# Kernel tuning notes

Hardware: AMD Instinct MI355X
Metric: run time of the kernel (lower is better)

## Reference

```python
import jax, jax.numpy as jnp
import numpy as np
import math

B, N, DIM, H, D, M = 2, 2048, 512, 8, 64, 128  # batch, seq, model dim, heads, head_dim, num_features


def _sample_orf(head_dim, num_features, seed=0):
    """Orthogonal random features with chi(d) norm scaling (FAVOR+), numpy host-side."""
    rng = np.random.default_rng(seed)
    blocks = []
    while len(blocks) * head_dim < num_features:
        G = rng.standard_normal((head_dim, head_dim)).astype(np.float32)
        Q, _ = np.linalg.qr(G)
        norms = np.linalg.norm(rng.standard_normal((head_dim, head_dim)).astype(np.float32), axis=1)
        blocks.append(np.diag(norms) @ Q.T)
    return np.concatenate(blocks, axis=0)[:num_features]


def setup_inputs() -> dict:
    key = jax.random.key(0)
    ks = jax.random.split(key, 6)
    inner = H * D
    x = jax.random.normal(ks[0], (B, N, DIM), dtype=jnp.float32)
    s = DIM ** -0.5
    Wq = jax.random.normal(ks[1], (inner, DIM), dtype=jnp.float32) * s
    Wk = jax.random.normal(ks[2], (inner, DIM), dtype=jnp.float32) * s
    Wv = jax.random.normal(ks[3], (inner, DIM), dtype=jnp.float32) * s
    Wo = jax.random.normal(ks[4], (DIM, inner), dtype=jnp.float32) * (inner ** -0.5)
    bo = jax.random.normal(ks[5], (DIM,), dtype=jnp.float32) * 0.01
    omega = jnp.asarray(_sample_orf(D, M), dtype=jnp.float32)  # [M, D]
    return {"x": x, "omega": omega, "Wq": Wq, "Wk": Wk, "Wv": Wv, "Wo": Wo, "bo": bo}


def _phi(x, omega, is_query):
    # x: [B,H,N,D], omega: [M,D] -> [B,H,N,M]
    proj = jnp.einsum('bhnd,md->bhnm', x, omega)
    log_phi = proj - 0.5 * jnp.sum(x * x, axis=-1, keepdims=True)
    if is_query:
        log_phi = log_phi - jnp.max(log_phi, axis=-1, keepdims=True)
    else:
        log_phi = log_phi - jnp.max(log_phi)
    return jnp.exp(log_phi) / math.sqrt(M) + 1e-4


def reference(x, omega, Wq, Wk, Wv, Wo, bo):
    # projections: torch Linear is y = x @ W.T
    q = (x @ Wq.T).reshape(B, N, H, D).transpose(0, 2, 1, 3)  # [B,H,N,D]
    k = (x @ Wk.T).reshape(B, N, H, D).transpose(0, 2, 1, 3)
    v = (x @ Wv.T).reshape(B, N, H, D).transpose(0, 2, 1, 3)
    scale = D ** -0.25
    phi_q = _phi(q * scale, omega, True)   # [B,H,N,M]
    phi_k = _phi(k * scale, omega, False)  # [B,H,N,M]

    # Causal linear attention as a recurrent scan over the sequence; math equals
    # cumsum of einsum('bhnm,bhnd->bhnmd') without the O(N*M*D) intermediate.
    def step(carry, inp):
        kv, ksum = carry                      # [B,H,M,D], [B,H,M]
        pqn, pkn, vn = inp                    # [B,H,M], [B,H,M], [B,H,D]
        kv = kv + pkn[..., None] * vn[:, :, None, :]
        ksum = ksum + pkn
        o = jnp.einsum('bhm,bhmd->bhd', pqn, kv)
        z = 1.0 / (jnp.einsum('bhm,bhm->bh', pqn, ksum) + 1e-6)
        return (kv, ksum), o * z[..., None]

    init = (jnp.zeros((B, H, M, D), x.dtype), jnp.zeros((B, H, M), x.dtype))
    xs = (phi_q.transpose(2, 0, 1, 3), phi_k.transpose(2, 0, 1, 3), v.transpose(2, 0, 1, 3))
    _, outs = jax.lax.scan(step, init, xs)    # outs: [N,B,H,D]
    out = outs.transpose(1, 0, 2, 3).reshape(B, N, H * D)
    return out @ Wo.T + bo
```

## Files before the change

### kernel.cpp

```cpp
#include <hip/hip_runtime.h>
#include <math.h>

#define B_ 2
#define N_ 2048
#define DIM_ 512
#define H_ 8
#define D_ 64
#define M_ 128
#define NC_ 32
#define C_ 64

#define INV_SQRT_M 0.08838834764831845f
#define QK_SCALE 0.35355339059327373f

typedef __attribute__((ext_vector_type(8))) short bf16x8;
typedef __attribute__((ext_vector_type(4))) short bf16x4;
typedef __attribute__((ext_vector_type(4))) float f32x4;

#define MFMA16(a, b, c) __builtin_amdgcn_mfma_f32_16x16x32_bf16((a), (b), (c), 0, 0, 0)

__device__ __forceinline__ short f2bf(float f) {
    union { float f; unsigned u; } x; x.f = f;
    unsigned r = (x.u + 0x7FFFu + ((x.u >> 16) & 1u)) >> 16;
    return (short)r;
}
__device__ __forceinline__ float bf2f(short s) {
    union { unsigned u; float f; } x; x.u = ((unsigned)(unsigned short)s) << 16;
    return x.f;
}
__device__ __forceinline__ unsigned encf(float f) {
    unsigned u = __float_as_uint(f);
    return (u & 0x80000000u) ? ~u : (u | 0x80000000u);
}
__device__ __forceinline__ float decf(unsigned e) {
    unsigned u = (e & 0x80000000u) ? (e & 0x7FFFFFFFu) : ~e;
    return __uint_as_float(u);
}

__device__ __forceinline__ void gl16(void* lds, const void* g) {
    __builtin_amdgcn_global_load_lds(
        (const __attribute__((address_space(1))) unsigned int*)g,
        (__attribute__((address_space(3))) unsigned int*)lds,
        16, 0, 0);
}

__device__ __forceinline__ bf16x8 ld_frag(const short* base, int row0, int k0, int ldk) {
    const int lane = threadIdx.x & 63;
    return *(const bf16x8*)(base + (row0 + (lane & 15)) * ldk + k0 + ((lane >> 4) << 3));
}
__device__ __forceinline__ bf16x8 ld_fragT(const short* base, int col0, int k0, int ldk) {
    const int lane = threadIdx.x & 63;
    const short* p = base + (k0 + ((lane >> 4) << 3)) * ldk + col0 + (lane & 15);
    bf16x8 r;
    #pragma unroll
    for (int i = 0; i < 8; ++i) r[i] = p[i * ldk];
    return r;
}

__global__ __launch_bounds__(256) void prep(
    const float* __restrict__ x, const float* __restrict__ Wq, const float* __restrict__ Wk,
    const float* __restrict__ Wv, const float* __restrict__ Wo,
    short* __restrict__ xh, short* __restrict__ xl,
    short* __restrict__ Wch, short* __restrict__ Woh, unsigned* __restrict__ gmaxu)
{
    int i4 = blockIdx.x * 256 + threadIdx.x;
    if (i4 == 0) gmaxu[0] = 0u;
    if (i4 < 524288) {
        float4 v = *(const float4*)(x + (size_t)i4 * 4);
        float a[4] = {v.x, v.y, v.z, v.w};
        bf16x4 hi, lo;
        #pragma unroll
        for (int u = 0; u < 4; ++u) {
            short h = f2bf(a[u]); hi[u] = h; lo[u] = f2bf(a[u] - bf2f(h));
        }
        *(bf16x4*)(xh + (size_t)i4 * 4) = hi;
        *(bf16x4*)(xl + (size_t)i4 * 4) = lo;
    } else {
        int r = i4 - 524288;
        int widx = r >> 16, off4 = r & 65535;
        const float* src; short* dst; float sc;
        if (widx == 0)      { src = Wq; dst = Wch;          sc = QK_SCALE; }
        else if (widx == 1) { src = Wk; dst = Wch + 262144; sc = QK_SCALE; }
        else if (widx == 2) { src = Wv; dst = Wch + 524288; sc = 1.f; }
        else                { src = Wo; dst = Woh;          sc = 1.f; }
        float4 v = *(const float4*)(src + (size_t)off4 * 4);
        bf16x4 hi;
        hi[0] = f2bf(v.x * sc); hi[1] = f2bf(v.y * sc);
        hi[2] = f2bf(v.z * sc); hi[3] = f2bf(v.w * sc);
        *(bf16x4*)(dst + (size_t)off4 * 4) = hi;
    }
}

__global__ __launch_bounds__(256) void prep_omw(const float* __restrict__ omega,
    const float* __restrict__ Wq, const float* __restrict__ Wk,
    short* __restrict__ Wch, short* __restrict__ Wcl)
{
    __shared__ float Ws[64][65];
    __shared__ float om[128][64];
    const int t = threadIdx.x;
    const int qk = blockIdx.x >> 6, h = (blockIdx.x >> 3) & 7, cb = blockIdx.x & 7;
    const int col0 = cb * 64;
    const float* W = qk ? Wk : Wq;
    for (int i = t; i < 64 * 64; i += 256) {
        int d = i >> 6, c = i & 63;
        Ws[d][c] = W[(size_t)(h * 64 + d) * 512 + col0 + c] * QK_SCALE;
    }
    for (int i = t; i < 128 * 64; i += 256) om[i >> 6][i & 63] = omega[i];
    __syncthreads();
    const int lane = t & 63, w = t >> 6;
    const int c = col0 + lane;
    float Wcol[64];
    #pragma unroll
    for (int d = 0; d < 64; ++d) Wcol[d] = Ws[d][lane];
    for (int mi = 0; mi < 32; ++mi) {
        int m = w * 32 + mi;
        float acc = 0.f;
        #pragma unroll
        for (int d = 0; d < 64; d += 4) {
            float4 o4 = *(const float4*)&om[m][d];
            acc += o4.x * Wcol[d] + o4.y * Wcol[d+1] + o4.z * Wcol[d+2] + o4.w * Wcol[d+3];
        }
        int row = 1536 + qk * 1024 + h * 128 + m;
        short hi = f2bf(acc);
        Wch[(size_t)row * 512 + c] = hi;
        Wcl[(size_t)row * 512 + c] = f2bf(acc - bf2f(hi));
    }
}

__global__ __launch_bounds__(256) void gemm_fused(
    const short* __restrict__ xh, const short* __restrict__ xl,
    const short* __restrict__ Wch, const short* __restrict__ Wcl,
    float* __restrict__ projq, float* __restrict__ projk,
    short* __restrict__ vbf, float* __restrict__ ssqbuf,
    float* __restrict__ qmaxp, float* __restrict__ pmaxp)
{
    __shared__ short Ah[128 * 32];
    __shared__ short Al[128 * 32];
    __shared__ short Bh[128 * 32];
    __shared__ short Bl[128 * 32];
    const int t = threadIdx.x, lane = t & 63, wave = t >> 6;
    const int wr = wave >> 1, wc = wave & 1;
    const int row0 = blockIdx.x * 128;
    const int by = blockIdx.y;
    const int col0 = by * 128;
    const int l_row = lane >> 2, l_col = (lane & 3) << 3;
    const bool three = (by >= 12);
    f32x4 acc[4][4];
    #pragma unroll
    for (int m = 0; m < 4; ++m)
        #pragma unroll
        for (int n = 0; n < 4; ++n) { f32x4 z = {0.f, 0.f, 0.f, 0.f}; acc[m][n] = z; }
    for (int k0 = 0; k0 < 512; k0 += 32) {
        #pragma unroll
        for (int sub = 0; sub < 2; ++sub) {
            int s = wave * 2 + sub;
            int gr = s * 16 + l_row;
            size_t ga = (size_t)(row0 + gr) * 512 + k0 + l_col;
            size_t gb = (size_t)(col0 + gr) * 512 + k0 + l_col;
            gl16(&Ah[s * 512], xh + ga);
            gl16(&Bh[s * 512], Wch + gb);
            if (three) {
                gl16(&Al[s * 512], xl + ga);
                gl16(&Bl[s * 512], Wcl + gb);
            }
        }
        __syncthreads();
        if (three) {
            bf16x8 bh[4], bl[4];
            #pragma unroll
            for (int n = 0; n < 4; ++n) {
                bh[n] = ld_frag(Bh, wc * 64 + n * 16, 0, 32);
                bl[n] = ld_frag(Bl, wc * 64 + n * 16, 0, 32);
            }
            #pragma unroll
            for (int m = 0; m < 4; ++m) {
                bf16x8 ah = ld_frag(Ah, wr * 64 + m * 16, 0, 32);
                bf16x8 al = ld_frag(Al, wr * 64 + m * 16, 0, 32);
                #pragma unroll
                for (int n = 0; n < 4; ++n) {
                    acc[m][n] = MFMA16(al, bh[n], acc[m][n]);
                    acc[m][n] = MFMA16(ah, bl[n], acc[m][n]);
                    acc[m][n] = MFMA16(ah, bh[n], acc[m][n]);
                }
            }
        } else {
            bf16x8 bh[4];
            #pragma unroll
            for (int n = 0; n < 4; ++n) bh[n] = ld_frag(Bh, wc * 64 + n * 16, 0, 32);
            #pragma unroll
            for (int m = 0; m < 4; ++m) {
                bf16x8 ah = ld_frag(Ah, wr * 64 + m * 16, 0, 32);
                #pragma unroll
                for (int n = 0; n < 4; ++n) acc[m][n] = MFMA16(ah, bh[n], acc[m][n]);
            }
        }
        __syncthreads();
    }
    if (by < 8) {
        const int qk = by >> 2;
        const int head = (by * 2 + wc) & 7;
        #pragma unroll
        for (int m = 0; m < 4; ++m)
            #pragma unroll
            for (int i = 0; i < 4; ++i) {
                float s = 0.f;
                #pragma unroll
                for (int n = 0; n < 4; ++n) { float v2 = acc[m][n][i]; s += v2 * v2; }
                s += __shfl_xor(s, 1); s += __shfl_xor(s, 2);
                s += __shfl_xor(s, 4); s += __shfl_xor(s, 8);
                if ((lane & 15) == 0) {
                    int row = row0 + wr * 64 + m * 16 + ((lane >> 4) << 2) + i;
                    int b = row >> 11, nn = row & 2047;
                    ssqbuf[qk * 32768 + (b * 8 + head) * 2048 + nn] = s;
                }
            }
    } else if (by < 12) {
        #pragma unroll
        for (int m = 0; m < 4; ++m)
            #pragma unroll
            for (int n = 0; n < 4; ++n)
                #pragma unroll
                for (int i = 0; i < 4; ++i) {
                    int row = row0 + wr * 64 + m * 16 + ((lane >> 4) << 2) + i;
                    int gc = col0 + wc * 64 + n * 16 + (lane & 15);
                    int c = gc - 1024, h = c >> 6, d = c & 63;
                    int b = row >> 11, nn = row & 2047;
                    vbf[((size_t)(b * 8 + h) * 2048 + nn) * 64 + d] = f2bf(acc[m][n][i]);
                }
    } else {
        float* dst = (by < 20) ? projq : projk;
        float* mdst = (by < 20) ? qmaxp : pmaxp;
        const int coff = (by < 20) ? 1536 : 2560;
        const int h = (by < 20) ? (by - 12) : (by - 20);
        #pragma unroll
        for (int m = 0; m < 4; ++m)
            #pragma unroll
            for (int n = 0; n < 4; ++n)
                #pragma unroll
                for (int i = 0; i < 4; ++i) {
                    int row = row0 + wr * 64 + m * 16 + ((lane >> 4) << 2) + i;
                    int pc = col0 - coff + wc * 64 + n * 16 + (lane & 15);
                    dst[(size_t)row * 1024 + pc] = acc[m][n][i];
                }
        #pragma unroll
        for (int m = 0; m < 4; ++m)
            #pragma unroll
            for (int i = 0; i < 4; ++i) {
                float mx = fmaxf(fmaxf(acc[m][0][i], acc[m][1][i]),
                                 fmaxf(acc[m][2][i], acc[m][3][i]));
                mx = fmaxf(mx, __shfl_xor(mx, 1));
                mx = fmaxf(mx, __shfl_xor(mx, 2));
                mx = fmaxf(mx, __shfl_xor(mx, 4));
                mx = fmaxf(mx, __shfl_xor(mx, 8));
                if ((lane & 15) == 0) {
                    int row = row0 + wr * 64 + m * 16 + ((lane >> 4) << 2) + i;
                    int b = row >> 11, nn = row & 2047;
                    size_t g = (size_t)(b * 8 + h) * 2048 + nn;
                    mdst[2 * g + wc] = mx;
                }
            }
    }
}

__global__ __launch_bounds__(256) void kmax_reduce(const float* __restrict__ pmaxp,
    const float* __restrict__ ssqbuf, unsigned* __restrict__ gmaxu)
{
    float m = -3.402823466e38f;
    for (int g = blockIdx.x * 256 + threadIdx.x; g < 32768; g += 8192)
        m = fmaxf(m, fmaxf(pmaxp[2 * g], pmaxp[2 * g + 1]) - 0.5f * ssqbuf[32768 + g]);
    #pragma unroll
    for (int off = 1; off < 64; off <<= 1) m = fmaxf(m, __shfl_xor(m, off));
    __shared__ float w[4];
    if ((threadIdx.x & 63) == 0) w[threadIdx.x >> 6] = m;
    __syncthreads();
    if (threadIdx.x == 0)
        atomicMax(gmaxu, encf(fmaxf(fmaxf(w[0], w[1]), fmaxf(w[2], w[3]))));
}

__global__ __launch_bounds__(256) void phi_q_ew(
    const float* __restrict__ projq, const float* __restrict__ qmaxp,
    short* __restrict__ phiq)
{
    size_t i4 = (size_t)blockIdx.x * 256 + threadIdx.x;
    size_t e = i4 * 4;
    int r = (int)(e >> 10), c = (int)(e & 1023);
    int h = c >> 7, m = c & 127;
    int b = r >> 11, n = r & 2047;
    int g = (b * 8 + h) * 2048 + n;
    float4 p = *(const float4*)(projq + e);
    float qm = fmaxf(qmaxp[2 * (size_t)g], qmaxp[2 * (size_t)g + 1]);
    bf16x4 o;
    o[0] = f2bf(expf(p.x - qm) * INV_SQRT_M + 1e-4f);
    o[1] = f2bf(expf(p.y - qm) * INV_SQRT_M + 1e-4f);
    o[2] = f2bf(expf(p.z - qm) * INV_SQRT_M + 1e-4f);
    o[3] = f2bf(expf(p.w - qm) * INV_SQRT_M + 1e-4f);
    *(bf16x4*)(phiq + (size_t)g * 128 + m) = o;
}

__global__ __launch_bounds__(256) void chunk_kv_mfma(
    const float* __restrict__ projk, const float* __restrict__ ssqbuf,
    const unsigned* __restrict__ gmaxu, const short* __restrict__ v_bf,
    short* __restrict__ phik, float* __restrict__ S, float* __restrict__ ksum)
{
    __shared__ short pk_l[64][136];
    __shared__ short v_l[64][72];
    const int t = threadIdx.x, lane = t & 63, wave = t >> 6;
    const int wr = wave >> 1, wc = wave & 1;
    const int bh = blockIdx.x >> 5, j = blockIdx.x & 31;
    const int b = bh >> 3, h = bh & 7;
    const int n0 = j << 6;
    const float g = decf(gmaxu[0]);
    #pragma unroll
    for (int it = 0; it < 8; ++it) {
        int e4 = t + it * 256;
        int r = e4 >> 5, c4 = (e4 & 31) << 2;
        float4 p = *(const float4*)(projk + ((size_t)(b * 2048 + n0 + r)) * 1024 + h * 128 + c4);
        float skv = 0.5f * ssqbuf[32768 + bh * 2048 + n0 + r];
        bf16x4 o;
        o[0] = f2bf(expf(p.x - skv - g) * INV_SQRT_M + 1e-4f);
        o[1] = f2bf(expf(p.y - skv - g) * INV_SQRT_M + 1e-4f);
        o[2] = f2bf(expf(p.z - skv - g) * INV_SQRT_M + 1e-4f);
        o[3] = f2bf(expf(p.w - skv - g) * INV_SQRT_M + 1e-4f);
        *(bf16x4*)&pk_l[r][c4] = o;
        *(bf16x4*)(phik + ((size_t)(bh * 2048 + n0 + r)) * 128 + c4) = o;
    }
    #pragma unroll
    for (int it = 0; it < 2; ++it) {
        int idx = t + it * 256;
        int r = idx >> 3, c8 = (idx & 7) << 3;
        *(bf16x8*)&v_l[r][c8] = *(const bf16x8*)(v_bf + ((size_t)(bh * 2048 + n0 + r)) * 64 + c8);
    }
    __syncthreads();
    f32x4 acc[2][4];
    #pragma unroll
    for (int mi = 0; mi < 2; ++mi)
        #pragma unroll
        for (int ni = 0; ni < 4; ++ni) { f32x4 z = {0.f, 0.f, 0.f, 0.f}; acc[mi][ni] = z; }
    #pragma unroll
    for (int ks = 0; ks < 2; ++ks) {
        bf16x8 a0 = ld_fragT(&v_l[0][0], wr * 32, ks * 32, 72);
        bf16x8 a1 = ld_fragT(&v_l[0][0], wr * 32 + 16, ks * 32, 72);
        #pragma unroll
        for (int ni = 0; ni < 4; ++ni) {
            bf16x8 bb = ld_fragT(&pk_l[0][0], wc * 64 + ni * 16, ks * 32, 136);
            acc[0][ni] = MFMA16(a0, bb, acc[0][ni]);
            acc[1][ni] = MFMA16(a1, bb, acc[1][ni]);
        }
    }
    const size_t sbase = ((size_t)blockIdx.x) << 13;
    #pragma unroll
    for (int mi = 0; mi < 2; ++mi)
        #pragma unroll
        for (int ni = 0; ni < 4; ++ni)
            #pragma unroll
            for (int i = 0; i < 4; ++i) {
                int row = wr * 32 + mi * 16 + ((lane >> 4) << 2) + i;
                int col = wc * 64 + ni * 16 + (lane & 15);
                S[sbase + (size_t)row * 128 + col] = acc[mi][ni][i];
            }
    if (t < 128) {
        float s = 0.f;
        #pragma unroll 8
        for (int n = 0; n < 64; ++n) s += bf2f(pk_l[n][t]);
        ksum[((size_t)blockIdx.x) * 128 + t] = s;
    }
}

__global__ __launch_bounds__(256) void prefix_scan(const float* __restrict__ S,
    const float* __restrict__ ksum, short* __restrict__ STbf, float* __restrict__ kpre)
{
    const int bh = blockIdx.x, y = blockIdx.y, t = threadIdx.x;
    if (y < 32) {
        int e = y * 256 + t;
        size_t base = (size_t)bh * NC_ * 8192 + e;
        float vals[NC_];
        #pragma unroll
        for (int j = 0; j < NC_; ++j) vals[j] = S[base + (size_t)j * 8192];
        float run = 0.f;
        #pragma unroll
        for (int j = 0; j < NC_; ++j) {
            STbf[base + (size_t)j * 8192] = f2bf(run);
            run += vals[j];
        }
    } else if (t < 128) {
        size_t base = (size_t)bh * NC_ * 128 + t;
        float vals[NC_];
        #pragma unroll
        for (int j = 0; j < NC_; ++j) vals[j] = ksum[base + (size_t)j * 128];
        float run = 0.f;
        #pragma unroll
        for (int j = 0; j < NC_; ++j) {
            kpre[base + (size_t)j * 128] = run;
            run += vals[j];
        }
    }
}

__global__ __launch_bounds__(256) void chunk_out_mfma(
    const short* __restrict__ phi_q, const short* __restrict__ phi_k,
    const short* __restrict__ v_bf, const short* __restrict__ STbf,
    const float* __restrict__ kpre, short* __restrict__ o_hi, short* __restrict__ o_lo)
{
    __shared__ short pq_l[64][136];
    __shared__ short pkst_l[64][136];
    __shared__ short v_l[64][72];
    __shared__ short a_l[64][72];
    __shared__ float rsum[64][8];
    __shared__ float den[64];
    __shared__ float ksp_l[128];
    const int t = threadIdx.x, lane = t & 63, wave = t >> 6;
    const int wr = wave >> 1, wc = wave & 1;
    const int bh = blockIdx.x >> 5, j = blockIdx.x & 31;
    const int n0 = j << 6;
    const size_t prow = (size_t)bh * N_ + n0;
    #pragma unroll
    for (int it = 0; it < 4; ++it) {
        int idx = t + it * 256;
        int r = idx >> 4, c8 = (idx & 15) << 3;
        *(bf16x8*)&pq_l[r][c8] = *(const bf16x8*)(phi_q + (prow + r) * 128 + c8);
        *(bf16x8*)&pkst_l[r][c8] = *(const bf16x8*)(phi_k + (prow + r) * 128 + c8);
    }
    #pragma unroll
    for (int it = 0; it < 2; ++it) {
        int idx = t + it * 256;
        int r = idx >> 3, c8 = (idx & 7) << 3;
        *(bf16x8*)&v_l[r][c8] = *(const bf16x8*)(v_bf + (prow + r) * 64 + c8);
    }
    if (t < 128) ksp_l[t] = kpre[((size_t)bh * NC_ + j) * 128 + t];
    __syncthreads();
    f32x4 qk[2][2];
    #pragma unroll
    for (int mi = 0; mi < 2; ++mi)
        #pragma unroll
        for (int ni = 0; ni < 2; ++ni) { f32x4 z = {0.f, 0.f, 0.f, 0.f}; qk[mi][ni] = z; }
    #pragma unroll
    for (int ks = 0; ks < 4; ++ks) {
        bf16x8 a0 = ld_frag(&pq_l[0][0], wr * 32, ks * 32, 136);
        bf16x8 a1 = ld_frag(&pq_l[0][0], wr * 32 + 16, ks * 32, 136);
        bf16x8 b0 = ld_frag(&pkst_l[0][0], wc * 32, ks * 32, 136);
        bf16x8 b1 = ld_frag(&pkst_l[0][0], wc * 32 + 16, ks * 32, 136);
        qk[0][0] = MFMA16(a0, b0, qk[0][0]);
        qk[0][1] = MFMA16(a0, b1, qk[0][1]);
        qk[1][0] = MFMA16(a1, b0, qk[1][0]);
        qk[1][1] = MFMA16(a1, b1, qk[1][1]);
    }
    #pragma unroll
    for (int mi = 0; mi < 2; ++mi)
        #pragma unroll
        for (int i = 0; i < 4; ++i) {
            int row = wr * 32 + mi * 16 + ((lane >> 4) << 2) + i;
            float part = 0.f;
            #pragma unroll
            for (int ni = 0; ni < 2; ++ni) {
                int col = wc * 32 + ni * 16 + (lane & 15);
                float val = (col <= row) ? qk[mi][ni][i] : 0.f;
                a_l[row][col] = f2bf(val);
                part += val;
            }
            part += __shfl_xor(part, 1);
            part += __shfl_xor(part, 2);
            part += __shfl_xor(part, 4);
            part += __shfl_xor(part, 8);
            if ((lane & 15) == 0) rsum[row][wc] = part;
        }
    {
        int row = t & 63, qq = t >> 6;
        float s = 0.f;
        #pragma unroll
        for (int m = 0; m < 32; ++m) s += bf2f(pq_l[row][qq * 32 + m]) * ksp_l[qq * 32 + m];
        rsum[row][4 + qq] = s;
    }
    __syncthreads();
    #pragma unroll
    for (int it = 0; it < 4; ++it) {
        int idx = t + it * 256;
        int r = idx >> 4, c8 = (idx & 15) << 3;
        *(bf16x8*)&pkst_l[r][c8] =
            *(const bf16x8*)(STbf + (((size_t)bh * NC_ + j) << 13) + r * 128 + c8);
    }
    if (t < 64) {
        float s = rsum[t][0] + rsum[t][1] + rsum[t][4] + rsum[t][5] + rsum[t][6] + rsum[t][7];
        den[t] = 1.0f / (s + 1e-6f);
    }
    __syncthreads();
    f32x4 oa[2][2];
    #pragma unroll
    for (int mi = 0; mi < 2; ++mi)
        #pragma unroll
        for (int ni = 0; ni < 2; ++ni) { f32x4 z = {0.f, 0.f, 0.f, 0.f}; oa[mi][ni] = z; }
    #pragma unroll
    for (int ks = 0; ks < 2; ++ks) {
        bf16x8 a0 = ld_frag(&a_l[0][0], wr * 32, ks * 32, 72);
        bf16x8 a1 = ld_frag(&a_l[0][0], wr * 32 + 16, ks * 32, 72);
        #pragma unroll
        for (int ni = 0; ni < 2; ++ni) {
            bf16x8 bb = ld_fragT(&v_l[0][0], wc * 32 + ni * 16, ks * 32, 72);
            oa[0][ni] = MFMA16(a0, bb, oa[0][ni]);
            oa[1][ni] = MFMA16(a1, bb, oa[1][ni]);
        }
    }
    #pragma unroll
    for (int ks = 0; ks < 4; ++ks) {
        bf16x8 a0 = ld_frag(&pq_l[0][0], wr * 32, ks * 32, 136);
        bf16x8 a1 = ld_frag(&pq_l[0][0], wr * 32 + 16, ks * 32, 136);
        #pragma unroll
        for (int ni = 0; ni < 2; ++ni) {
            bf16x8 bb = ld_frag(&pkst_l[0][0], wc * 32 + ni * 16, ks * 32, 136);
            oa[0][ni] = MFMA16(a0, bb, oa[0][ni]);
            oa[1][ni] = MFMA16(a1, bb, oa[1][ni]);
        }
    }
    const int b_ = bh >> 3, h = bh & 7;
    #pragma unroll
    for (int mi = 0; mi < 2; ++mi)
        #pragma unroll
        for (int ni = 0; ni < 2; ++ni)
            #pragma unroll
            for (int i = 0; i < 4; ++i) {
                int row = wr * 32 + mi * 16 + ((lane >> 4) << 2) + i;
                int col = wc * 32 + ni * 16 + (lane & 15);
                float val = oa[mi][ni][i] * den[row];
                size_t oi = ((size_t)b_ * N_ + n0 + row) * 512 + h * 64 + col;
                short hi = f2bf(val);
                o_hi[oi] = hi;
                o_lo[oi] = f2bf(val - bf2f(hi));
            }
}

__global__ __launch_bounds__(256) void gemm_out(
    const short* __restrict__ ohi, const short* __restrict__ olo,
    const short* __restrict__ Woh, const float* __restrict__ bo, float* __restrict__ out)
{
    __shared__ short Ah[128 * 32];
    __shared__ short Al[128 * 32];
    __shared__ short Bh[64 * 32];
    const int t = threadIdx.x, lane = t & 63, wave = t >> 6;
    const int row0 = blockIdx.x * 128, col0 = blockIdx.y * 64;
    const int l_row = lane >> 2, l_col = (lane & 3) << 3;
    f32x4 acc[2][4];
    #pragma unroll
    for (int m = 0; m < 2; ++m)
        #pragma unroll
        for (int n = 0; n < 4; ++n) { f32x4 z = {0.f, 0.f, 0.f, 0.f}; acc[m][n] = z; }
    for (int k0 = 0; k0 < 512; k0 += 32) {
        #pragma unroll
        for (int sub = 0; sub < 2; ++sub) {
            int s = wave * 2 + sub;
            int gr = s * 16 + l_row;
            size_t ga = (size_t)(row0 + gr) * 512 + k0 + l_col;
            gl16(&Ah[s * 512], ohi + ga);
            gl16(&Al[s * 512], olo + ga);
        }
        {
            int gr = wave * 16 + l_row;
            size_t gb = (size_t)(col0 + gr) * 512 + k0 + l_col;
            gl16(&Bh[wave * 512], Woh + gb);
        }
        __syncthreads();
        bf16x8 bh[4];
        #pragma unroll
        for (int n = 0; n < 4; ++n) bh[n] = ld_frag(Bh, n * 16, 0, 32);
        #pragma unroll
        for (int m = 0; m < 2; ++m) {
            bf16x8 ah = ld_frag(Ah, wave * 32 + m * 16, 0, 32);
            bf16x8 al = ld_frag(Al, wave * 32 + m * 16, 0, 32);
            #pragma unroll
            for (int n = 0; n < 4; ++n) {
                acc[m][n] = MFMA16(al, bh[n], acc[m][n]);
                acc[m][n] = MFMA16(ah, bh[n], acc[m][n]);
            }
        }
        __syncthreads();
    }
    #pragma unroll
    for (int m = 0; m < 2; ++m)
        #pragma unroll
        for (int n = 0; n < 4; ++n)
            #pragma unroll
            for (int i = 0; i < 4; ++i) {
                int gr = row0 + wave * 32 + m * 16 + ((lane >> 4) << 2) + i;
                int gc = col0 + n * 16 + (lane & 15);
                out[(size_t)gr * 512 + gc] = acc[m][n][i] + bo[gc];
            }
}

extern "C" void kernel_launch(void* const* d_in, const int* in_sizes, int n_in,
                              void* d_out, int out_size, void* d_ws, size_t ws_size,
                              hipStream_t stream) {
    const float* x     = (const float*)d_in[0];
    const float* omega = (const float*)d_in[1];
    const float* Wq    = (const float*)d_in[2];
    const float* Wk    = (const float*)d_in[3];
    const float* Wv    = (const float*)d_in[4];
    const float* Wo    = (const float*)d_in[5];
    const float* bo    = (const float*)d_in[6];
    float* out = (float*)d_out;

    char* w = (char*)d_ws;
    short* xh   = (short*)(w);
    short* xl   = (short*)(w + (4ull  << 20));
    short* Wch  = (short*)(w + (8ull  << 20));
    short* Wcl  = (short*)(w + (11ull << 20) + (512ull << 10));
    short* Woh  = (short*)(w + (16ull << 20));
    float* projq= (float*)(w + (17ull << 20));
    float* projk= (float*)(w + (33ull << 20));
    short* vbf  = (short*)(w + (49ull << 20));
    short* STbf = (short*)(w + (53ull << 20));
    short* ohi  = (short*)(w + (61ull << 20));
    short* olo  = (short*)(w + (65ull << 20));
    float* ssqb = (float*)(w + (69ull << 20));
    float* ksum = (float*)(w + (69ull << 20) + (256ull << 10));
    float* kpre = (float*)(w + (69ull << 20) + (512ull << 10));
    float* pmaxp= (float*)(w + (69ull << 20) + (768ull << 10));
    float* qmaxp= (float*)(w + (70ull << 20));
    unsigned* gmaxu = (unsigned*)(w + (70ull << 20) + (256ull << 10));
    short* phiq = (short*)(w);
    short* phik = (short*)(w + (8ull << 20));
    float* S    = projq;

    prep<<<3072, 256, 0, stream>>>(x, Wq, Wk, Wv, Wo, xh, xl, Wch, Woh, gmaxu);
    prep_omw<<<128, 256, 0, stream>>>(omega, Wq, Wk, Wch, Wcl);
    gemm_fused<<<dim3(32, 28), 256, 0, stream>>>(xh, xl, Wch, Wcl, projq, projk,
                                                 vbf, ssqb, qmaxp, pmaxp);
    kmax_reduce<<<32, 256, 0, stream>>>(pmaxp, ssqb, gmaxu);
    phi_q_ew<<<4096, 256, 0, stream>>>(projq, qmaxp, phiq);
    chunk_kv_mfma<<<512, 256, 0, stream>>>(projk, ssqb, gmaxu, vbf, phik, S, ksum);
    prefix_scan<<<dim3(16, 33), 256, 0, stream>>>(S, ksum, STbf, kpre);
    chunk_out_mfma<<<512, 256, 0, stream>>>(phiq, phik, vbf, STbf, kpre, ohi, olo);
    gemm_out<<<dim3(32, 8), 256, 0, stream>>>(ohi, olo, Woh, bo, out);
}
```

Measured before the change: 182.8 us.

## Fuse phi exponentials into projection GEMM epilogue and drop plain Q projection

The fused GEMM no longer computes the plain q projection, since only its omega-folded form is needed for phi_q. Its epilogue now applies the row-max exponential directly and writes bf16 phi_q and a per-row-normalised phi_k instead of fp32 projections, which removes the phi_q_ew kernel and the large fp32 intermediate traffic. The global key max is applied later as a per-row scale when phi_k is loaded in the chunk kernels, and the chunk KV states are stored as bf16. The rescale of an already-rounded bf16 value and the bf16 chunk states add rounding error in exchange for less memory traffic.

```diff
diff --git a/kernel.cpp b/kernel.cpp
--- a/kernel.cpp
+++ b/kernel.cpp
@@ -58,8 +58,8 @@
 }
 
 __global__ __launch_bounds__(256) void prep(
-    const float* __restrict__ x, const float* __restrict__ Wq, const float* __restrict__ Wk,
-    const float* __restrict__ Wv, const float* __restrict__ Wo,
+    const float* __restrict__ x, const float* __restrict__ Wk, const float* __restrict__ Wv,
+    const float* __restrict__ Wo,
     short* __restrict__ xh, short* __restrict__ xl,
     short* __restrict__ Wch, short* __restrict__ Woh, unsigned* __restrict__ gmaxu)
 {
@@ -75,13 +75,12 @@
         }
         *(bf16x4*)(xh + (size_t)i4 * 4) = hi;
         *(bf16x4*)(xl + (size_t)i4 * 4) = lo;
-    } else {
+    } else if (i4 < 720896) {
         int r = i4 - 524288;
         int widx = r >> 16, off4 = r & 65535;
         const float* src; short* dst; float sc;
-        if (widx == 0)      { src = Wq; dst = Wch;          sc = QK_SCALE; }
-        else if (widx == 1) { src = Wk; dst = Wch + 262144; sc = QK_SCALE; }
-        else if (widx == 2) { src = Wv; dst = Wch + 524288; sc = 1.f; }
+        if (widx == 0)      { src = Wk; dst = Wch;          sc = QK_SCALE; }
+        else if (widx == 1) { src = Wv; dst = Wch + 262144; sc = 1.f; }
         else                { src = Wo; dst = Woh;          sc = 1.f; }
         float4 v = *(const float4*)(src + (size_t)off4 * 4);
         bf16x4 hi;
@@ -120,7 +119,7 @@
             float4 o4 = *(const float4*)&om[m][d];
             acc += o4.x * Wcol[d] + o4.y * Wcol[d+1] + o4.z * Wcol[d+2] + o4.w * Wcol[d+3];
         }
-        int row = 1536 + qk * 1024 + h * 128 + m;
+        int row = 1024 + qk * 1024 + h * 128 + m;
         short hi = f2bf(acc);
         Wch[(size_t)row * 512 + c] = hi;
         Wcl[(size_t)row * 512 + c] = f2bf(acc - bf2f(hi));
@@ -130,21 +129,21 @@
 __global__ __launch_bounds__(256) void gemm_fused(
     const short* __restrict__ xh, const short* __restrict__ xl,
     const short* __restrict__ Wch, const short* __restrict__ Wcl,
-    float* __restrict__ projq, float* __restrict__ projk,
-    short* __restrict__ vbf, float* __restrict__ ssqbuf,
-    float* __restrict__ qmaxp, float* __restrict__ pmaxp)
+    short* __restrict__ phiq, short* __restrict__ pkloc,
+    short* __restrict__ vbf, float* __restrict__ ssqbuf, float* __restrict__ pmaxp)
 {
     __shared__ short Ah[128 * 32];
     __shared__ short Al[128 * 32];
     __shared__ short Bh[128 * 32];
     __shared__ short Bl[128 * 32];
+    __shared__ float rmx[128][2];
     const int t = threadIdx.x, lane = t & 63, wave = t >> 6;
     const int wr = wave >> 1, wc = wave & 1;
     const int row0 = blockIdx.x * 128;
     const int by = blockIdx.y;
     const int col0 = by * 128;
     const int l_row = lane >> 2, l_col = (lane & 3) << 3;
-    const bool three = (by >= 12);
+    const bool three = (by >= 8);
     f32x4 acc[4][4];
     #pragma unroll
     for (int m = 0; m < 4; ++m)
@@ -196,9 +195,8 @@
         }
         __syncthreads();
     }
-    if (by < 8) {
-        const int qk = by >> 2;
-        const int head = (by * 2 + wc) & 7;
+    if (by < 4) {
+        const int head = by * 2 + wc;
         #pragma unroll
         for (int m = 0; m < 4; ++m)
             #pragma unroll
@@ -211,10 +209,10 @@
                 if ((lane & 15) == 0) {
                     int row = row0 + wr * 64 + m * 16 + ((lane >> 4) << 2) + i;
                     int b = row >> 11, nn = row & 2047;
-                    ssqbuf[qk * 32768 + (b * 8 + head) * 2048 + nn] = s;
+                    ssqbuf[(b * 8 + head) * 2048 + nn] = s;
                 }
             }
-    } else if (by < 12) {
+    } else if (by < 8) {
         #pragma unroll
         for (int m = 0; m < 4; ++m)
             #pragma unroll
@@ -223,25 +221,13 @@
                 for (int i = 0; i < 4; ++i) {
                     int row = row0 + wr * 64 + m * 16 + ((lane >> 4) << 2) + i;
                     int gc = col0 + wc * 64 + n * 16 + (lane & 15);
-                    int c = gc - 1024, h = c >> 6, d = c & 63;
+                    int c = gc - 512, h = c >> 6, d = c & 63;
                     int b = row >> 11, nn = row & 2047;
                     vbf[((size_t)(b * 8 + h) * 2048 + nn) * 64 + d] = f2bf(acc[m][n][i]);
                 }
     } else {
-        float* dst = (by < 20) ? projq : projk;
-        float* mdst = (by < 20) ? qmaxp : pmaxp;
-        const int coff = (by < 20) ? 1536 : 2560;
-        const int h = (by < 20) ? (by - 12) : (by - 20);
-        #pragma unroll
-        for (int m = 0; m < 4; ++m)
-            #pragma unroll
-            for (int n = 0; n < 4; ++n)
-                #pragma unroll
-                for (int i = 0; i < 4; ++i) {
-                    int row = row0 + wr * 64 + m * 16 + ((lane >> 4) << 2) + i;
-                    int pc = col0 - coff + wc * 64 + n * 16 + (lane & 15);
-                    dst[(size_t)row * 1024 + pc] = acc[m][n][i];
-                }
+        const bool isq = (by < 16);
+        const int h = isq ? (by - 8) : (by - 16);
         #pragma unroll
         for (int m = 0; m < 4; ++m)
             #pragma unroll
@@ -252,12 +238,28 @@
                 mx = fmaxf(mx, __shfl_xor(mx, 2));
                 mx = fmaxf(mx, __shfl_xor(mx, 4));
                 mx = fmaxf(mx, __shfl_xor(mx, 8));
-                if ((lane & 15) == 0) {
-                    int row = row0 + wr * 64 + m * 16 + ((lane >> 4) << 2) + i;
-                    int b = row >> 11, nn = row & 2047;
-                    size_t g = (size_t)(b * 8 + h) * 2048 + nn;
-                    mdst[2 * g + wc] = mx;
+                if ((lane & 15) == 0)
+                    rmx[wr * 64 + m * 16 + ((lane >> 4) << 2) + i][wc] = mx;
+            }
+        __syncthreads();
+        short* dst = isq ? phiq : pkloc;
+        #pragma unroll
+        for (int m = 0; m < 4; ++m)
+            #pragma unroll
+            for (int i = 0; i < 4; ++i) {
+                int lr = wr * 64 + m * 16 + ((lane >> 4) << 2) + i;
+                float fm = fmaxf(rmx[lr][0], rmx[lr][1]);
+                int row = row0 + lr;
+                int b = row >> 11, nn = row & 2047;
+                size_t g = (size_t)(b * 8 + h) * 2048 + nn;
+                #pragma unroll
+                for (int n = 0; n < 4; ++n) {
+                    int mc = wc * 64 + n * 16 + (lane & 15);
+                    float e = expf(acc[m][n][i] - fm);
+                    float val = isq ? (e * INV_SQRT_M + 1e-4f) : e;
+                    dst[g * 128 + mc] = f2bf(val);
                 }
+                if (!isq && wc == 0 && (lane & 15) == 0) pmaxp[g] = fm;
             }
     }
 }
@@ -267,7 +269,7 @@
 {
     float m = -3.402823466e38f;
     for (int g = blockIdx.x * 256 + threadIdx.x; g < 32768; g += 8192)
-        m = fmaxf(m, fmaxf(pmaxp[2 * g], pmaxp[2 * g + 1]) - 0.5f * ssqbuf[32768 + g]);
+        m = fmaxf(m, pmaxp[g] - 0.5f * ssqbuf[g]);
     #pragma unroll
     for (int off = 1; off < 64; off <<= 1) m = fmaxf(m, __shfl_xor(m, off));
     __shared__ float w[4];
@@ -277,52 +279,34 @@
         atomicMax(gmaxu, encf(fmaxf(fmaxf(w[0], w[1]), fmaxf(w[2], w[3]))));
 }
 
-__global__ __launch_bounds__(256) void phi_q_ew(
-    const float* __restrict__ projq, const float* __restrict__ qmaxp,
-    short* __restrict__ phiq)
-{
-    size_t i4 = (size_t)blockIdx.x * 256 + threadIdx.x;
-    size_t e = i4 * 4;
-    int r = (int)(e >> 10), c = (int)(e & 1023);
-    int h = c >> 7, m = c & 127;
-    int b = r >> 11, n = r & 2047;
-    int g = (b * 8 + h) * 2048 + n;
-    float4 p = *(const float4*)(projq + e);
-    float qm = fmaxf(qmaxp[2 * (size_t)g], qmaxp[2 * (size_t)g + 1]);
-    bf16x4 o;
-    o[0] = f2bf(expf(p.x - qm) * INV_SQRT_M + 1e-4f);
-    o[1] = f2bf(expf(p.y - qm) * INV_SQRT_M + 1e-4f);
-    o[2] = f2bf(expf(p.z - qm) * INV_SQRT_M + 1e-4f);
-    o[3] = f2bf(expf(p.w - qm) * INV_SQRT_M + 1e-4f);
-    *(bf16x4*)(phiq + (size_t)g * 128 + m) = o;
-}
-
 __global__ __launch_bounds__(256) void chunk_kv_mfma(
-    const float* __restrict__ projk, const float* __restrict__ ssqbuf,
-    const unsigned* __restrict__ gmaxu, const short* __restrict__ v_bf,
-    short* __restrict__ phik, float* __restrict__ S, float* __restrict__ ksum)
+    const short* __restrict__ pkloc, const float* __restrict__ ssqbuf,
+    const float* __restrict__ pmaxp, const unsigned* __restrict__ gmaxu,
+    const short* __restrict__ v_bf, short* __restrict__ Sbf, float* __restrict__ ksum)
 {
     __shared__ short pk_l[64][136];
     __shared__ short v_l[64][72];
+    __shared__ float srow[64];
     const int t = threadIdx.x, lane = t & 63, wave = t >> 6;
     const int wr = wave >> 1, wc = wave & 1;
     const int bh = blockIdx.x >> 5, j = blockIdx.x & 31;
-    const int b = bh >> 3, h = bh & 7;
     const int n0 = j << 6;
     const float g = decf(gmaxu[0]);
-    #pragma unroll
-    for (int it = 0; it < 8; ++it) {
-        int e4 = t + it * 256;
-        int r = e4 >> 5, c4 = (e4 & 31) << 2;
-        float4 p = *(const float4*)(projk + ((size_t)(b * 2048 + n0 + r)) * 1024 + h * 128 + c4);
-        float skv = 0.5f * ssqbuf[32768 + bh * 2048 + n0 + r];
-        bf16x4 o;
-        o[0] = f2bf(expf(p.x - skv - g) * INV_SQRT_M + 1e-4f);
-        o[1] = f2bf(expf(p.y - skv - g) * INV_SQRT_M + 1e-4f);
-        o[2] = f2bf(expf(p.z - skv - g) * INV_SQRT_M + 1e-4f);
-        o[3] = f2bf(expf(p.w - skv - g) * INV_SQRT_M + 1e-4f);
-        *(bf16x4*)&pk_l[r][c4] = o;
-        *(bf16x4*)(phik + ((size_t)(bh * 2048 + n0 + r)) * 128 + c4) = o;
+    if (t < 64) {
+        int gr = bh * 2048 + n0 + t;
+        srow[t] = expf(pmaxp[gr] - 0.5f * ssqbuf[gr] - g) * INV_SQRT_M;
+    }
+    __syncthreads();
+    #pragma unroll
+    for (int it = 0; it < 4; ++it) {
+        int idx = t + it * 256;
+        int r = idx >> 4, c8 = (idx & 15) << 3;
+        bf16x8 raw = *(const bf16x8*)(pkloc + ((size_t)(bh * 2048 + n0 + r)) * 128 + c8);
+        float s = srow[r];
+        bf16x8 o;
+        #pragma unroll
+        for (int u = 0; u < 8; ++u) o[u] = f2bf(bf2f(raw[u]) * s + 1e-4f);
+        *(bf16x8*)&pk_l[r][c8] = o;
     }
     #pragma unroll
     for (int it = 0; it < 2; ++it) {
@@ -356,7 +340,7 @@
             for (int i = 0; i < 4; ++i) {
                 int row = wr * 32 + mi * 16 + ((lane >> 4) << 2) + i;
                 int col = wc * 64 + ni * 16 + (lane & 15);
-                S[sbase + (size_t)row * 128 + col] = acc[mi][ni][i];
+                Sbf[sbase + (size_t)row * 128 + col] = f2bf(acc[mi][ni][i]);
             }
     if (t < 128) {
         float s = 0.f;
@@ -366,7 +350,7 @@
     }
 }
 
-__global__ __launch_bounds__(256) void prefix_scan(const float* __restrict__ S,
+__global__ __launch_bounds__(256) void prefix_scan(const short* __restrict__ Sbf,
     const float* __restrict__ ksum, short* __restrict__ STbf, float* __restrict__ kpre)
 {
     const int bh = blockIdx.x, y = blockIdx.y, t = threadIdx.x;
@@ -375,7 +359,7 @@
         size_t base = (size_t)bh * NC_ * 8192 + e;
         float vals[NC_];
         #pragma unroll
-        for (int j = 0; j < NC_; ++j) vals[j] = S[base + (size_t)j * 8192];
+        for (int j = 0; j < NC_; ++j) vals[j] = bf2f(Sbf[base + (size_t)j * 8192]);
         float run = 0.f;
         #pragma unroll
         for (int j = 0; j < NC_; ++j) {
@@ -397,7 +381,9 @@
 }
 
 __global__ __launch_bounds__(256) void chunk_out_mfma(
-    const short* __restrict__ phi_q, const short* __restrict__ phi_k,
+    const short* __restrict__ phi_q, const short* __restrict__ pkloc,
+    const float* __restrict__ ssqbuf, const float* __restrict__ pmaxp,
+    const unsigned* __restrict__ gmaxu,
     const short* __restrict__ v_bf, const short* __restrict__ STbf,
     const float* __restrict__ kpre, short* __restrict__ o_hi, short* __restrict__ o_lo)
 {
@@ -408,17 +394,30 @@
     __shared__ float rsum[64][8];
     __shared__ float den[64];
     __shared__ float ksp_l[128];
+    __shared__ float srow[64];
     const int t = threadIdx.x, lane = t & 63, wave = t >> 6;
     const int wr = wave >> 1, wc = wave & 1;
     const int bh = blockIdx.x >> 5, j = blockIdx.x & 31;
     const int n0 = j << 6;
     const size_t prow = (size_t)bh * N_ + n0;
+    const float g = decf(gmaxu[0]);
+    if (t < 64) {
+        int gr = bh * 2048 + n0 + t;
+        srow[t] = expf(pmaxp[gr] - 0.5f * ssqbuf[gr] - g) * INV_SQRT_M;
+    }
+    if (t < 128) ksp_l[t] = kpre[((size_t)bh * NC_ + j) * 128 + t];
+    __syncthreads();
     #pragma unroll
     for (int it = 0; it < 4; ++it) {
         int idx = t + it * 256;
         int r = idx >> 4, c8 = (idx & 15) << 3;
         *(bf16x8*)&pq_l[r][c8] = *(const bf16x8*)(phi_q + (prow + r) * 128 + c8);
-        *(bf16x8*)&pkst_l[r][c8] = *(const bf16x8*)(phi_k + (prow + r) * 128 + c8);
+        bf16x8 raw = *(const bf16x8*)(pkloc + (prow + r) * 128 + c8);
+        float s = srow[r];
+        bf16x8 o;
+        #pragma unroll
+        for (int u = 0; u < 8; ++u) o[u] = f2bf(bf2f(raw[u]) * s + 1e-4f);
+        *(bf16x8*)&pkst_l[r][c8] = o;
     }
     #pragma unroll
     for (int it = 0; it < 2; ++it) {
@@ -426,7 +425,6 @@
         int r = idx >> 3, c8 = (idx & 7) << 3;
         *(bf16x8*)&v_l[r][c8] = *(const bf16x8*)(v_bf + (prow + r) * 64 + c8);
     }
-    if (t < 128) ksp_l[t] = kpre[((size_t)bh * NC_ + j) * 128 + t];
     __syncthreads();
     f32x4 qk[2][2];
     #pragma unroll
@@ -600,32 +598,29 @@
     short* xh   = (short*)(w);
     short* xl   = (short*)(w + (4ull  << 20));
     short* Wch  = (short*)(w + (8ull  << 20));
-    short* Wcl  = (short*)(w + (11ull << 20) + (512ull << 10));
-    short* Woh  = (short*)(w + (16ull << 20));
-    float* projq= (float*)(w + (17ull << 20));
-    float* projk= (float*)(w + (33ull << 20));
-    short* vbf  = (short*)(w + (49ull << 20));
-    short* STbf = (short*)(w + (53ull << 20));
-    short* ohi  = (short*)(w + (61ull << 20));
-    short* olo  = (short*)(w + (65ull << 20));
-    float* ssqb = (float*)(w + (69ull << 20));
-    float* ksum = (float*)(w + (69ull << 20) + (256ull << 10));
-    float* kpre = (float*)(w + (69ull << 20) + (512ull << 10));
-    float* pmaxp= (float*)(w + (69ull << 20) + (768ull << 10));
-    float* qmaxp= (float*)(w + (70ull << 20));
-    unsigned* gmaxu = (unsigned*)(w + (70ull << 20) + (256ull << 10));
-    short* phiq = (short*)(w);
-    short* phik = (short*)(w + (8ull << 20));
-    float* S    = projq;
-
-    prep<<<3072, 256, 0, stream>>>(x, Wq, Wk, Wv, Wo, xh, xl, Wch, Woh, gmaxu);
+    short* Wcl  = (short*)(w + (11ull << 20));
+    short* Woh  = (short*)(w + (14ull << 20));
+    short* phiq = (short*)(w + (15ull << 20));
+    short* pkloc= (short*)(w + (23ull << 20));
+    short* vbf  = (short*)(w + (31ull << 20));
+    short* Sbf  = (short*)(w + (35ull << 20));
+    short* STbf = (short*)(w + (43ull << 20));
+    short* ohi  = (short*)(w + (51ull << 20));
+    short* olo  = (short*)(w + (55ull << 20));
+    float* ssqb = (float*)(w + (59ull << 20));
+    float* pmaxp= (float*)(w + (59ull << 20) + (128ull << 10));
+    float* ksum = (float*)(w + (59ull << 20) + (256ull << 10));
+    float* kpre = (float*)(w + (59ull << 20) + (512ull << 10));
+    unsigned* gmaxu = (unsigned*)(w + (59ull << 20) + (768ull << 10));
+
+    prep<<<2816, 256, 0, stream>>>(x, Wk, Wv, Wo, xh, xl, Wch, Woh, gmaxu);
     prep_omw<<<128, 256, 0, stream>>>(omega, Wq, Wk, Wch, Wcl);
-    gemm_fused<<<dim3(32, 28), 256, 0, stream>>>(xh, xl, Wch, Wcl, projq, projk,
-                                                 vbf, ssqb, qmaxp, pmaxp);
+    gemm_fused<<<dim3(32, 24), 256, 0, stream>>>(xh, xl, Wch, Wcl, phiq, pkloc,
+                                                 vbf, ssqb, pmaxp);
     kmax_reduce<<<32, 256, 0, stream>>>(pmaxp, ssqb, gmaxu);
-    phi_q_ew<<<4096, 256, 0, stream>>>(projq, qmaxp, phiq);
-    chunk_kv_mfma<<<512, 256, 0, stream>>>(projk, ssqb, gmaxu, vbf, phik, S, ksum);
-    prefix_scan<<<dim3(16, 33), 256, 0, stream>>>(S, ksum, STbf, kpre);
-    chunk_out_mfma<<<512, 256, 0, stream>>>(phiq, phik, vbf, STbf, kpre, ohi, olo);
+    chunk_kv_mfma<<<512, 256, 0, stream>>>(pkloc, ssqb, pmaxp, gmaxu, vbf, Sbf, ksum);
+    prefix_scan<<<dim3(16, 33), 256, 0, stream>>>(Sbf, ksum, STbf, kpre);
+    chunk_out_mfma<<<512, 256, 0, stream>>>(phiq, pkloc, ssqb, pmaxp, gmaxu,
+                                            vbf, STbf, kpre, ohi, olo);
     gemm_out<<<dim3(32, 8), 256, 0, stream>>>(ohi, olo, Woh, bo, out);
 }
```

New measurement: 173.6 us. 5.1% less time.
